# Kernel tuning notes

Hardware: AMD Instinct MI355X
Metric: run time of the kernel (lower is better)

## Reference

```python
import jax, jax.numpy as jnp
import numpy as np

B, E, H = 16384, 768, 8
HD = E // H
EPS = 1e-5


def layernorm(x, g, b):
    m = jnp.mean(x, axis=-1, keepdims=True)
    v = jnp.mean((x - m) ** 2, axis=-1, keepdims=True)
    return (x - m) * jax.lax.rsqrt(v + EPS) * g + b


def mha1(q_in, kv_in, Wq, bq, Wk, bk, Wv, bv, Wo, bo):
    # seq_len-1 cross attention: softmax over a single key is identically 1
    Bn = q_in.shape[0]
    q = (q_in @ Wq.T + bq).reshape(Bn, H, HD)
    k = (kv_in @ Wk.T + bk).reshape(Bn, H, HD)
    v = (kv_in @ Wv.T + bv).reshape(Bn, H, HD)
    scores = jnp.sum(q * k, axis=-1) / (HD ** 0.5)      # [B, H]
    w = jax.nn.softmax(scores[..., None], axis=-1)       # [B, H, 1] == 1
    ctx = (w * v).reshape(Bn, E)
    return ctx @ Wo.T + bo


def ffn(x, W1, b1, W2, b2):
    return jax.nn.gelu(x @ W1.T + b1, approximate=False) @ W2.T + b2


def setup_inputs() -> dict:
    key = jax.random.key(0)
    ks = iter(jax.random.split(key, 40))
    s = 0.02
    d = {
        "image_embed": jax.random.normal(next(ks), (B, E), jnp.float32),
        "text_embed": jax.random.normal(next(ks), (B, E), jnp.float32),
    }
    for p in ("it", "ti"):
        for w in ("Wq", "Wk", "Wv", "Wo"):
            d[f"{p}_{w}"] = jax.random.normal(next(ks), (E, E), jnp.float32) * s
        for bname in ("bq", "bk", "bv", "bo"):
            d[f"{p}_{bname}"] = jnp.zeros((E,), jnp.float32)
    for p in ("ln_img", "ln_text", "fp_ln"):
        d[f"{p}_g"] = jnp.ones((E,), jnp.float32)
        d[f"{p}_b"] = jnp.zeros((E,), jnp.float32)
    for p in ("fi", "ft"):
        d[f"{p}_W1"] = jax.random.normal(next(ks), (4 * E, E), jnp.float32) * s
        d[f"{p}_b1"] = jnp.zeros((4 * E,), jnp.float32)
        d[f"{p}_W2"] = jax.random.normal(next(ks), (E, 4 * E), jnp.float32) * s
        d[f"{p}_b2"] = jnp.zeros((E,), jnp.float32)
    d["fp_W"] = jax.random.normal(next(ks), (E, 2 * E), jnp.float32) * s
    d["fp_b"] = jnp.zeros((E,), jnp.float32)
    return d


def reference(image_embed, text_embed,
              it_Wq, it_Wk, it_Wv, it_Wo, it_bq, it_bk, it_bv, it_bo,
              ti_Wq, ti_Wk, ti_Wv, ti_Wo, ti_bq, ti_bk, ti_bv, ti_bo,
              ln_img_g, ln_img_b, ln_text_g, ln_text_b, fp_ln_g, fp_ln_b,
              fi_W1, fi_b1, fi_W2, fi_b2, ft_W1, ft_b1, ft_W2, ft_b2,
              fp_W, fp_b):
    img_att = mha1(image_embed, text_embed, it_Wq, it_bq, it_Wk, it_bk, it_Wv, it_bv, it_Wo, it_bo)
    img = layernorm(image_embed + img_att, ln_img_g, ln_img_b)
    img = img + ffn(img, fi_W1, fi_b1, fi_W2, fi_b2)
    txt_att = mha1(text_embed, img, ti_Wq, ti_bq, ti_Wk, ti_bk, ti_Wv, ti_bv, ti_Wo, ti_bo)
    txt = layernorm(text_embed + txt_att, ln_text_g, ln_text_b)
    txt = txt + ffn(txt, ft_W1, ft_b1, ft_W2, ft_b2)
    fused = jnp.concatenate([img, txt], axis=-1)
    return jax.nn.gelu(layernorm(fused @ fp_W.T + fp_b, fp_ln_g, fp_ln_b), approximate=False)
```

## Files before the change

### kernel.cpp

```cpp
#include <hip/hip_runtime.h>
#include <hip/hip_bf16.h>
#include <math.h>


typedef unsigned short u16;
typedef __bf16 bf16_t;
typedef bf16_t bf16x8 __attribute__((ext_vector_type(8)));
typedef float f32x4 __attribute__((ext_vector_type(4)));

#define BROWS 16384
#define EDIM  768

__device__ __forceinline__ u16 f2bf(float f) {
    union { float f; unsigned u; } v; v.f = f;
    return (u16)((v.u + 0x7FFFu + ((v.u >> 16) & 1u)) >> 16);
}
__device__ __forceinline__ float bf2f(u16 h) {
    union { unsigned u; float f; } v; v.u = ((unsigned)h) << 16;
    return v.f;
}
__device__ __forceinline__ float gelu_f(float x) {
    float t = x * x;
    float p = fmaf(0.102943268f, t, 2.30221895f);
    float e = __builtin_amdgcn_exp2f(-x * p);
    return x * __builtin_amdgcn_rcpf(1.0f + e);
}

__device__ __forceinline__ void gld16(const u16* g, u16* l) {
    __builtin_amdgcn_global_load_lds(
        (__attribute__((address_space(1))) void*)g,
        (__attribute__((address_space(3))) void*)l, 16, 0, 0);
}

struct ConvBatch {
    const float *s0, *s1, *s2, *s3, *s4, *s5, *s6, *s7;
    u16 *d0, *d1, *d2, *d3, *d4, *d5, *d6, *d7;
};
#define CB0 2304
#define CB1 2304
#define CB2 2304
#define CB3 2304
#define CB4 1152
#define CB5 576
#define CB6 576
#define CB7 12288
#define CONV_BLOCKS (CB0+CB1+CB2+CB3+CB4+CB5+CB6+CB7)

__global__ void __launch_bounds__(256) conv8_k(ConvBatch cb) {
    int b = blockIdx.x;
    const float* s; u16* d;
    if      (b < CB0)          { s = cb.s0; d = cb.d0; }
    else if ((b -= CB0) < CB1) { s = cb.s1; d = cb.d1; }
    else if ((b -= CB1) < CB2) { s = cb.s2; d = cb.d2; }
    else if ((b -= CB2) < CB3) { s = cb.s3; d = cb.d3; }
    else if ((b -= CB3) < CB4) { s = cb.s4; d = cb.d4; }
    else if ((b -= CB4) < CB5) { s = cb.s5; d = cb.d5; }
    else if ((b -= CB5) < CB6) { s = cb.s6; d = cb.d6; }
    else    { b -= CB6;          s = cb.s7; d = cb.d7; }
    int i = b * 256 + threadIdx.x;
    float4 v = ((const float4*)s)[i];
    ushort4 o;
    o.x = f2bf(v.x); o.y = f2bf(v.y); o.z = f2bf(v.z); o.w = f2bf(v.w);
    ((ushort4*)d)[i] = o;
}

__global__ void __launch_bounds__(256) f32_to_bf16_T_k(const float* __restrict__ S,
                                                       u16* __restrict__ D,
                                                       int R, int C) {
    __shared__ float t[32][33];
    const int r0 = blockIdx.y * 32, c0 = blockIdx.x * 32;
    const int tx = threadIdx.x & 31, ty = threadIdx.x >> 5;
#pragma unroll
    for (int i = ty; i < 32; i += 8) t[i][tx] = S[(long)(r0 + i) * C + c0 + tx];
    __syncthreads();
#pragma unroll
    for (int i = ty; i < 32; i += 8) D[(long)(c0 + i) * R + r0 + tx] = f2bf(t[tx][i]);
}

__global__ void __launch_bounds__(256) bias_comb_k(const float* __restrict__ Wo,
                                                   const float* __restrict__ bv,
                                                   const float* __restrict__ bo,
                                                   float* __restrict__ bc, int K) {
    const int n = blockIdx.x * 4 + (threadIdx.x >> 6);
    const int lane = threadIdx.x & 63;
    float s = 0.f;
    for (int k = lane; k < K; k += 64) s += Wo[(long)n * K + k] * bv[k];
#pragma unroll
    for (int o = 32; o > 0; o >>= 1) s += __shfl_down(s, o, 64);
    if (lane == 0) bc[n] = s + bo[n];
}

__global__ void __launch_bounds__(512, 2) gemm_bt(
    const u16* __restrict__ A, int lda,
    const u16* __restrict__ W,
    const float* __restrict__ bias,
    const float* __restrict__ R, int ldr,
    const u16* __restrict__ Rb, int ldrb,
    float* __restrict__ Cf, int ldcf,
    u16* __restrict__ Cb, int ldcb,
    int K, int do_gelu)
{
    __shared__ alignas(16) u16 sA[4][256 * 32];
    __shared__ alignas(16) u16 sB[4][256 * 32];

    const int tid  = threadIdx.x;
    const int lane = tid & 63;
    const int wave = tid >> 6;
    const int wm = wave >> 2;
    const int wn = wave & 3;

    int bm, bn;
    {
        const int gx = gridDim.x, gy = gridDim.y;
        const int id = blockIdx.y * gx + blockIdx.x;
        if ((gy & 7) == 0) {
            const int xcd = id & 7, slot = id >> 3;
            bn = slot % gx;
            bm = (xcd * (gy >> 3)) + slot / gx;
        } else { bm = blockIdx.y; bn = blockIdx.x; }
    }
    const long m0 = (long)bm * 256;
    const long n0 = (long)bn * 256;

    const int srow = lane >> 2;
    const int sk   = ((lane & 3) ^ ((lane >> 3) & 3)) * 8;
    const u16* gA = A + (m0 + wave * 16 + srow) * (long)lda + sk;
    const u16* gB = W + (n0 + wave * 16 + srow) * (long)K + sk;
    const long rdA2 = 128 * (long)lda;
    const long rdB2 = 128 * (long)K;

#define STA(sl, t, ks) do { const u16* g_ = gA + (t) * 64 + (ks) * 32; \
    gld16(g_,        &sA[sl][wave * 512]); \
    gld16(g_ + rdA2, &sA[sl][4096 + wave * 512]); } while (0)
#define STB(sl, t, ks) do { const u16* g_ = gB + (t) * 64 + (ks) * 32; \
    gld16(g_,        &sB[sl][wave * 512]); \
    gld16(g_ + rdB2, &sB[sl][4096 + wave * 512]); } while (0)

    const int quad = lane >> 4;
    const int l16  = lane & 15;
    const int koff = (quad ^ ((l16 >> 1) & 3)) << 4;
    __attribute__((address_space(3))) const u16* baseA3 =
        (__attribute__((address_space(3))) const u16*)
        ((const char*)&sA[0][0] + wm * 8192 + l16 * 64 + koff);
    __attribute__((address_space(3))) const u16* baseB3 =
        (__attribute__((address_space(3))) const u16*)
        ((const char*)&sB[0][0] + wn * 4096 + l16 * 64 + koff);

    f32x4 acc[8][4];
#pragma unroll
    for (int i = 0; i < 8; i++)
#pragma unroll
        for (int j = 0; j < 4; j++) {
            f32x4 z = {0.f, 0.f, 0.f, 0.f};
            acc[i][j] = z;
        }
    bf16x8 af0, af1, af2, af3, bf0, bf1, bf2, bf3;

#define DSR(dst, base, off) \
    asm volatile("ds_read_b128 %0, %1 offset:%2" \
                 : "=v"(dst) : "v"(base), "i"(off))
#define VM4   asm volatile("s_waitcnt vmcnt(4)" ::: "memory")
#define NOWAIT ((void)0)

#define PHASE(SLA, MQ, LB, SLB, STG, WAIT) do {                              \
    DSR(af0, baseA3, (SLA) * 16384 + (MQ) * 4096 + 0);                       \
    DSR(af1, baseA3, (SLA) * 16384 + (MQ) * 4096 + 1024);                    \
    DSR(af2, baseA3, (SLA) * 16384 + (MQ) * 4096 + 2048);                    \
    DSR(af3, baseA3, (SLA) * 16384 + (MQ) * 4096 + 3072);                    \
    if (LB) {                                                                \
        DSR(bf0, baseB3, (SLB) * 16384 + 0);                                 \
        DSR(bf1, baseB3, (SLB) * 16384 + 1024);                              \
        DSR(bf2, baseB3, (SLB) * 16384 + 2048);                              \
        DSR(bf3, baseB3, (SLB) * 16384 + 3072);                              \
    }                                                                        \
    STG;                                                                     \
    WAIT;                                                                    \
    __builtin_amdgcn_sched_barrier(0);                                       \
    __builtin_amdgcn_s_barrier();                                            \
    asm volatile("s_waitcnt lgkmcnt(0)" ::: "memory");                       \
    __builtin_amdgcn_sched_barrier(0);                                       \
    __builtin_amdgcn_s_setprio(1);                                           \
    acc[(MQ)*4+0][0] = __builtin_amdgcn_mfma_f32_16x16x32_bf16(af0, bf0, acc[(MQ)*4+0][0], 0, 0, 0); \
    acc[(MQ)*4+0][1] = __builtin_amdgcn_mfma_f32_16x16x32_bf16(af0, bf1, acc[(MQ)*4+0][1], 0, 0, 0); \
    acc[(MQ)*4+0][2] = __builtin_amdgcn_mfma_f32_16x16x32_bf16(af0, bf2, acc[(MQ)*4+0][2], 0, 0, 0); \
    acc[(MQ)*4+0][3] = __builtin_amdgcn_mfma_f32_16x16x32_bf16(af0, bf3, acc[(MQ)*4+0][3], 0, 0, 0); \
    acc[(MQ)*4+1][0] = __builtin_amdgcn_mfma_f32_16x16x32_bf16(af1, bf0, acc[(MQ)*4+1][0], 0, 0, 0); \
    acc[(MQ)*4+1][1] = __builtin_amdgcn_mfma_f32_16x16x32_bf16(af1, bf1, acc[(MQ)*4+1][1], 0, 0, 0); \
    acc[(MQ)*4+1][2] = __builtin_amdgcn_mfma_f32_16x16x32_bf16(af1, bf2, acc[(MQ)*4+1][2], 0, 0, 0); \
    acc[(MQ)*4+1][3] = __builtin_amdgcn_mfma_f32_16x16x32_bf16(af1, bf3, acc[(MQ)*4+1][3], 0, 0, 0); \
    acc[(MQ)*4+2][0] = __builtin_amdgcn_mfma_f32_16x16x32_bf16(af2, bf0, acc[(MQ)*4+2][0], 0, 0, 0); \
    acc[(MQ)*4+2][1] = __builtin_amdgcn_mfma_f32_16x16x32_bf16(af2, bf1, acc[(MQ)*4+2][1], 0, 0, 0); \
    acc[(MQ)*4+2][2] = __builtin_amdgcn_mfma_f32_16x16x32_bf16(af2, bf2, acc[(MQ)*4+2][2], 0, 0, 0); \
    acc[(MQ)*4+2][3] = __builtin_amdgcn_mfma_f32_16x16x32_bf16(af2, bf3, acc[(MQ)*4+2][3], 0, 0, 0); \
    acc[(MQ)*4+3][0] = __builtin_amdgcn_mfma_f32_16x16x32_bf16(af3, bf0, acc[(MQ)*4+3][0], 0, 0, 0); \
    acc[(MQ)*4+3][1] = __builtin_amdgcn_mfma_f32_16x16x32_bf16(af3, bf1, acc[(MQ)*4+3][1], 0, 0, 0); \
    acc[(MQ)*4+3][2] = __builtin_amdgcn_mfma_f32_16x16x32_bf16(af3, bf2, acc[(MQ)*4+3][2], 0, 0, 0); \
    acc[(MQ)*4+3][3] = __builtin_amdgcn_mfma_f32_16x16x32_bf16(af3, bf3, acc[(MQ)*4+3][3], 0, 0, 0); \
    __builtin_amdgcn_s_setprio(0);                                           \
    __builtin_amdgcn_sched_barrier(0);                                       \
    __builtin_amdgcn_s_barrier();                                            \
  } while (0)

    const int nt = K >> 6;
    STA(0, 0, 0); STB(0, 0, 0);
    STA(1, 0, 1); STB(1, 0, 1);
    STA(2, 1, 0); STB(2, 1, 0);
    VM4;
    __builtin_amdgcn_s_barrier();

    for (int T = 0; T < nt; T += 2) {
        const int t2 = (T + 2 < nt) ? T + 2 : 0;
        const int t3 = (T + 3 < nt) ? T + 3 : 1;
        PHASE(0, 0, 1, 0, STA(3, T + 1, 1), NOWAIT);
        PHASE(0, 1, 0, 0, STB(3, T + 1, 1), VM4);
        PHASE(1, 0, 1, 1, STA(0, t2, 0),    NOWAIT);
        PHASE(1, 1, 0, 1, STB(0, t2, 0),    NOWAIT);
        PHASE(2, 0, 1, 2, STA(1, t2, 1),    NOWAIT);
        PHASE(2, 1, 0, 2, STB(1, t2, 1),    VM4);
        PHASE(3, 0, 1, 3, STA(2, t3, 0),    NOWAIT);
        PHASE(3, 1, 0, 3, STB(2, t3, 0),    NOWAIT);
    }

#pragma unroll
    for (int mt = 0; mt < 8; mt++) {
#pragma unroll
        for (int nf = 0; nf < 4; nf++) {
            const long col = n0 + wn * 64 + nf * 16 + l16;
            const float bv = bias ? bias[col] : 0.0f;
#pragma unroll
            for (int rr = 0; rr < 4; rr++) {
                const long row = m0 + wm * 128 + mt * 16 + quad * 4 + rr;
                float v = acc[mt][nf][rr] + bv;
                if (R)  v += R[row * (long)ldr + col];
                if (Rb) v += bf2f(Rb[row * (long)ldrb + col]);
                if (do_gelu) v = gelu_f(v);
                if (Cf) Cf[row * (long)ldcf + col] = v;
                if (Cb) Cb[row * (long)ldcb + col] = f2bf(v);
            }
        }
    }
#undef PHASE
#undef DSR
#undef STA
#undef STB
#undef VM4
#undef NOWAIT
}

__global__ void __launch_bounds__(256) ln_k(
    const u16*  __restrict__ Xb,
    const float* __restrict__ Xf,
    const float* __restrict__ g,
    const float* __restrict__ b,
    float* __restrict__ Yf,
    u16*   __restrict__ Yb,
    int do_gelu)
{
    const int row = blockIdx.x;
    const int tid = threadIdx.x;
    float v[4] = {0.f, 0.f, 0.f, 0.f};
    if (tid < 192) {
        if (Xb) {
            ushort4 u = ((const ushort4*)(Xb + (long)row * EDIM))[tid];
            v[0] = bf2f(u.x); v[1] = bf2f(u.y); v[2] = bf2f(u.z); v[3] = bf2f(u.w);
        } else {
            float4 f = ((const float4*)(Xf + (long)row * EDIM))[tid];
            v[0] = f.x; v[1] = f.y; v[2] = f.z; v[3] = f.w;
        }
    }
    float s = 0.f, s2 = 0.f;
#pragma unroll
    for (int j = 0; j < 4; j++) { s += v[j]; s2 += v[j] * v[j]; }
#pragma unroll
    for (int o = 32; o > 0; o >>= 1) {
        s  += __shfl_down(s,  o, 64);
        s2 += __shfl_down(s2, o, 64);
    }
    __shared__ float red[8];
    __shared__ float mb[2];
    const int wave = tid >> 6, lane = tid & 63;
    if (lane == 0) { red[wave] = s; red[4 + wave] = s2; }
    __syncthreads();
    if (tid == 0) {
        float S  = red[0] + red[1] + red[2] + red[3];
        float S2 = red[4] + red[5] + red[6] + red[7];
        float mean = S * (1.0f / 768.0f);
        float var  = S2 * (1.0f / 768.0f) - mean * mean;
        mb[0] = mean;
        mb[1] = rsqrtf(var + 1e-5f);
    }
    __syncthreads();
    if (tid < 192) {
        const float mean = mb[0], inv = mb[1];
        float y[4];
#pragma unroll
        for (int j = 0; j < 4; j++) {
            const int c = tid * 4 + j;
            y[j] = (v[j] - mean) * inv * g[c] + b[c];
            if (do_gelu) y[j] = gelu_f(y[j]);
        }
        if (Yf) {
            float4 o = {y[0], y[1], y[2], y[3]};
            ((float4*)(Yf + (long)row * EDIM))[tid] = o;
        }
        if (Yb) {
            ushort4 o = {f2bf(y[0]), f2bf(y[1]), f2bf(y[2]), f2bf(y[3])};
            ((ushort4*)(Yb + (long)row * EDIM))[tid] = o;
        }
    }
}

extern "C" void kernel_launch(void* const* d_in, const int* in_sizes, int n_in,
                              void* d_out, int out_size, void* d_ws, size_t ws_size,
                              hipStream_t stream) {
    (void)in_sizes; (void)n_in; (void)out_size;
    const float* image    = (const float*)d_in[0];
    const float* text     = (const float*)d_in[1];
    const float* it_Wv    = (const float*)d_in[4];
    const float* it_Wo    = (const float*)d_in[5];
    const float* it_bv    = (const float*)d_in[8];
    const float* it_bo    = (const float*)d_in[9];
    const float* ti_Wv    = (const float*)d_in[12];
    const float* ti_Wo    = (const float*)d_in[13];
    const float* ti_bv    = (const float*)d_in[16];
    const float* ti_bo    = (const float*)d_in[17];
    const float* ln_img_g = (const float*)d_in[18];
    const float* ln_img_b = (const float*)d_in[19];
    const float* ln_txt_g = (const float*)d_in[20];
    const float* ln_txt_b = (const float*)d_in[21];
    const float* fp_ln_g  = (const float*)d_in[22];
    const float* fp_ln_b  = (const float*)d_in[23];
    const float* fi_W1    = (const float*)d_in[24];
    const float* fi_b1    = (const float*)d_in[25];
    const float* fi_W2    = (const float*)d_in[26];
    const float* fi_b2    = (const float*)d_in[27];
    const float* ft_W1    = (const float*)d_in[28];
    const float* ft_b1    = (const float*)d_in[29];
    const float* ft_W2    = (const float*)d_in[30];
    const float* ft_b2    = (const float*)d_in[31];
    const float* fp_W     = (const float*)d_in[32];
    const float* fp_b     = (const float*)d_in[33];

    char* ws = (char*)d_ws;
    size_t off = 0;
    auto alloc = [&](size_t bytes) {
        char* p = ws + off; off += (bytes + 255) & ~(size_t)255; return p;
    };
    u16* wo_it = (u16*)alloc((size_t)768 * 768 * 2);
    u16* wvT_it= (u16*)alloc((size_t)768 * 768 * 2);
    u16* wc_it = (u16*)alloc((size_t)768 * 768 * 2);
    u16* wo_ti = (u16*)alloc((size_t)768 * 768 * 2);
    u16* wvT_ti= (u16*)alloc((size_t)768 * 768 * 2);
    u16* wc_ti = (u16*)alloc((size_t)768 * 768 * 2);
    u16* w1i   = (u16*)alloc((size_t)3072 * 768 * 2);
    u16* w2i   = (u16*)alloc((size_t)768 * 3072 * 2);
    u16* w1t   = (u16*)alloc((size_t)3072 * 768 * 2);
    u16* w2t   = (u16*)alloc((size_t)768 * 3072 * 2);
    u16* wp    = (u16*)alloc((size_t)768 * 1536 * 2);
    float* bc_it = (float*)alloc(768 * 4);
    float* bc_ti = (float*)alloc(768 * 4);
    u16* vbuf  = (u16*)alloc((size_t)BROWS * 768 * 2);
    u16* fused = (u16*)alloc((size_t)BROWS * 1536 * 2);
    u16* text_bf = fused;
    int fch = 16384;
    while (fch > 2048 && off + (size_t)fch * 3072 * 2 > ws_size) fch >>= 1;
    size_t region = (size_t)fch * 3072 * 2;
    if (region < (size_t)BROWS * 768 * 2) region = (size_t)BROWS * 768 * 2;
    u16* hbuf = (u16*)alloc(region);
    u16* pbuf = hbuf;

    auto gemm = [&](const u16* A, int lda, const u16* W, int M, int N, int K,
                    const float* bias, const float* R, int ldr,
                    const u16* Rb, int ldrb,
                    float* Cf, int ldcf, u16* Cb, int ldcb, int dg) {
        gemm_bt<<<dim3(N / 256, M / 256), dim3(512), 0, stream>>>(
            A, lda, W, bias, R, ldr, Rb, ldrb, Cf, ldcf, Cb, ldcb, K, dg);
    };
    auto ffn = [&](const u16* xin, const u16* W1, const float* b1,
                   const u16* W2, const float* b2, u16* outp, int ldout) {
        for (int c = 0; c < BROWS / fch; c++) {
            const u16* xc = xin + (size_t)c * fch * 768;
            gemm(xc, 768, W1, fch, 3072, 768, b1,
                 nullptr, 0, nullptr, 0, nullptr, 0, hbuf, 3072, 1);
            gemm(hbuf, 3072, W2, fch, 768, 3072, b2,
                 nullptr, 0, xc, 768,
                 nullptr, 0, outp + (size_t)c * fch * ldout, ldout, 0);
        }
    };

    ConvBatch cbt = { fi_W1, fi_W2, ft_W1, ft_W2, fp_W, it_Wo, ti_Wo, text,
                      w1i,   w2i,   w1t,   w2t,   wp,   wo_it, wo_ti, text_bf };
    conv8_k<<<dim3(CONV_BLOCKS), dim3(256), 0, stream>>>(cbt);
    f32_to_bf16_T_k<<<dim3(24, 24), dim3(256), 0, stream>>>(it_Wv, wvT_it, 768, 768);
    gemm(wo_it, 768, wvT_it, 768, 768, 768, nullptr,
         nullptr, 0, nullptr, 0, nullptr, 0, wc_it, 768, 0);
    bias_comb_k<<<dim3(192), dim3(256), 0, stream>>>(it_Wo, it_bv, it_bo, bc_it, 768);
    f32_to_bf16_T_k<<<dim3(24, 24), dim3(256), 0, stream>>>(ti_Wv, wvT_ti, 768, 768);
    gemm(wo_ti, 768, wvT_ti, 768, 768, 768, nullptr,
         nullptr, 0, nullptr, 0, nullptr, 0, wc_ti, 768, 0);
    bias_comb_k<<<dim3(192), dim3(256), 0, stream>>>(ti_Wo, ti_bv, ti_bo, bc_ti, 768);

    gemm(text_bf, 768, wc_it, BROWS, 768, 768, bc_it,
         image, 768, nullptr, 0, nullptr, 0, pbuf, 768, 0);
    ln_k<<<dim3(BROWS), dim3(256), 0, stream>>>(
        pbuf, nullptr, ln_img_g, ln_img_b, nullptr, vbuf, 0);
    ffn(vbuf, w1i, fi_b1, w2i, fi_b2, fused, 1536);
    gemm(fused, 1536, wc_ti, BROWS, 768, 768, bc_ti,
         text, 768, nullptr, 0, nullptr, 0, pbuf, 768, 0);
    ln_k<<<dim3(BROWS), dim3(256), 0, stream>>>(
        pbuf, nullptr, ln_txt_g, ln_txt_b, nullptr, vbuf, 0);
    ffn(vbuf, w1t, ft_b1, w2t, ft_b2, fused + 768, 1536);
    gemm(fused, 1536, wp, BROWS, 768, 1536, fp_b,
         nullptr, 0, nullptr, 0, nullptr, 0, pbuf, 768, 0);
    ln_k<<<dim3(BROWS), dim3(256), 0, stream>>>(
        pbuf, nullptr, fp_ln_g, fp_ln_b, (float*)d_out, nullptr, 1);
}
```

Before: 1.094 ms.

## Double-buffer LDS fragment registers to overlap ds_reads with MFMA

Restructures the GEMM main loop so the LDS fragment reads for the next phase are issued before the MFMAs of the current phase. Two register sets alternate, and the lgkmcnt/vmcnt waits are partial. Each phase now has one barrier instead of two, which is meant to hide LDS read latency behind matrix math. The cost is higher VGPR pressure from doubled fragment registers, which could lower occupancy. The finer waitcnt accounting also carries a correctness risk if the counts are off.

```diff
diff --git a/kernel.cpp b/kernel.cpp
--- a/kernel.cpp
+++ b/kernel.cpp
@@ -154,72 +154,83 @@
             f32x4 z = {0.f, 0.f, 0.f, 0.f};
             acc[i][j] = z;
         }
-    bf16x8 af0, af1, af2, af3, bf0, bf1, bf2, bf3;
+    bf16x8 a0_0, a0_1, a0_2, a0_3;
+    bf16x8 a1_0, a1_1, a1_2, a1_3;
+    bf16x8 b0_0, b0_1, b0_2, b0_3;
+    bf16x8 b1_0, b1_1, b1_2, b1_3;
 
 #define DSR(dst, base, off) \
     asm volatile("ds_read_b128 %0, %1 offset:%2" \
                  : "=v"(dst) : "v"(base), "i"(off))
-#define VM4   asm volatile("s_waitcnt vmcnt(4)" ::: "memory")
-#define NOWAIT ((void)0)
-
-#define PHASE(SLA, MQ, LB, SLB, STG, WAIT) do {                              \
-    DSR(af0, baseA3, (SLA) * 16384 + (MQ) * 4096 + 0);                       \
-    DSR(af1, baseA3, (SLA) * 16384 + (MQ) * 4096 + 1024);                    \
-    DSR(af2, baseA3, (SLA) * 16384 + (MQ) * 4096 + 2048);                    \
-    DSR(af3, baseA3, (SLA) * 16384 + (MQ) * 4096 + 3072);                    \
-    if (LB) {                                                                \
-        DSR(bf0, baseB3, (SLB) * 16384 + 0);                                 \
-        DSR(bf1, baseB3, (SLB) * 16384 + 1024);                              \
-        DSR(bf2, baseB3, (SLB) * 16384 + 2048);                              \
-        DSR(bf3, baseB3, (SLB) * 16384 + 3072);                              \
-    }                                                                        \
-    STG;                                                                     \
-    WAIT;                                                                    \
-    __builtin_amdgcn_sched_barrier(0);                                       \
-    __builtin_amdgcn_s_barrier();                                            \
-    asm volatile("s_waitcnt lgkmcnt(0)" ::: "memory");                       \
-    __builtin_amdgcn_sched_barrier(0);                                       \
-    __builtin_amdgcn_s_setprio(1);                                           \
-    acc[(MQ)*4+0][0] = __builtin_amdgcn_mfma_f32_16x16x32_bf16(af0, bf0, acc[(MQ)*4+0][0], 0, 0, 0); \
-    acc[(MQ)*4+0][1] = __builtin_amdgcn_mfma_f32_16x16x32_bf16(af0, bf1, acc[(MQ)*4+0][1], 0, 0, 0); \
-    acc[(MQ)*4+0][2] = __builtin_amdgcn_mfma_f32_16x16x32_bf16(af0, bf2, acc[(MQ)*4+0][2], 0, 0, 0); \
-    acc[(MQ)*4+0][3] = __builtin_amdgcn_mfma_f32_16x16x32_bf16(af0, bf3, acc[(MQ)*4+0][3], 0, 0, 0); \
-    acc[(MQ)*4+1][0] = __builtin_amdgcn_mfma_f32_16x16x32_bf16(af1, bf0, acc[(MQ)*4+1][0], 0, 0, 0); \
-    acc[(MQ)*4+1][1] = __builtin_amdgcn_mfma_f32_16x16x32_bf16(af1, bf1, acc[(MQ)*4+1][1], 0, 0, 0); \
-    acc[(MQ)*4+1][2] = __builtin_amdgcn_mfma_f32_16x16x32_bf16(af1, bf2, acc[(MQ)*4+1][2], 0, 0, 0); \
-    acc[(MQ)*4+1][3] = __builtin_amdgcn_mfma_f32_16x16x32_bf16(af1, bf3, acc[(MQ)*4+1][3], 0, 0, 0); \
-    acc[(MQ)*4+2][0] = __builtin_amdgcn_mfma_f32_16x16x32_bf16(af2, bf0, acc[(MQ)*4+2][0], 0, 0, 0); \
-    acc[(MQ)*4+2][1] = __builtin_amdgcn_mfma_f32_16x16x32_bf16(af2, bf1, acc[(MQ)*4+2][1], 0, 0, 0); \
-    acc[(MQ)*4+2][2] = __builtin_amdgcn_mfma_f32_16x16x32_bf16(af2, bf2, acc[(MQ)*4+2][2], 0, 0, 0); \
-    acc[(MQ)*4+2][3] = __builtin_amdgcn_mfma_f32_16x16x32_bf16(af2, bf3, acc[(MQ)*4+2][3], 0, 0, 0); \
-    acc[(MQ)*4+3][0] = __builtin_amdgcn_mfma_f32_16x16x32_bf16(af3, bf0, acc[(MQ)*4+3][0], 0, 0, 0); \
-    acc[(MQ)*4+3][1] = __builtin_amdgcn_mfma_f32_16x16x32_bf16(af3, bf1, acc[(MQ)*4+3][1], 0, 0, 0); \
-    acc[(MQ)*4+3][2] = __builtin_amdgcn_mfma_f32_16x16x32_bf16(af3, bf2, acc[(MQ)*4+3][2], 0, 0, 0); \
-    acc[(MQ)*4+3][3] = __builtin_amdgcn_mfma_f32_16x16x32_bf16(af3, bf3, acc[(MQ)*4+3][3], 0, 0, 0); \
-    __builtin_amdgcn_s_setprio(0);                                           \
-    __builtin_amdgcn_sched_barrier(0);                                       \
-    __builtin_amdgcn_s_barrier();                                            \
+#define RDA(S, SLA, MQ) do { \
+    DSR(a##S##_0, baseA3, (SLA) * 16384 + (MQ) * 4096 + 0);    \
+    DSR(a##S##_1, baseA3, (SLA) * 16384 + (MQ) * 4096 + 1024); \
+    DSR(a##S##_2, baseA3, (SLA) * 16384 + (MQ) * 4096 + 2048); \
+    DSR(a##S##_3, baseA3, (SLA) * 16384 + (MQ) * 4096 + 3072); \
   } while (0)
+#define RDB(S, SLB) do { \
+    DSR(b##S##_0, baseB3, (SLB) * 16384 + 0);    \
+    DSR(b##S##_1, baseB3, (SLB) * 16384 + 1024); \
+    DSR(b##S##_2, baseB3, (SLB) * 16384 + 2048); \
+    DSR(b##S##_3, baseB3, (SLB) * 16384 + 3072); \
+  } while (0)
+
+#define MM16(AS, BS, MQ) do { \
+    acc[(MQ)*4+0][0] = __builtin_amdgcn_mfma_f32_16x16x32_bf16(a##AS##_0, b##BS##_0, acc[(MQ)*4+0][0], 0, 0, 0); \
+    acc[(MQ)*4+0][1] = __builtin_amdgcn_mfma_f32_16x16x32_bf16(a##AS##_0, b##BS##_1, acc[(MQ)*4+0][1], 0, 0, 0); \
+    acc[(MQ)*4+0][2] = __builtin_amdgcn_mfma_f32_16x16x32_bf16(a##AS##_0, b##BS##_2, acc[(MQ)*4+0][2], 0, 0, 0); \
+    acc[(MQ)*4+0][3] = __builtin_amdgcn_mfma_f32_16x16x32_bf16(a##AS##_0, b##BS##_3, acc[(MQ)*4+0][3], 0, 0, 0); \
+    acc[(MQ)*4+1][0] = __builtin_amdgcn_mfma_f32_16x16x32_bf16(a##AS##_1, b##BS##_0, acc[(MQ)*4+1][0], 0, 0, 0); \
+    acc[(MQ)*4+1][1] = __builtin_amdgcn_mfma_f32_16x16x32_bf16(a##AS##_1, b##BS##_1, acc[(MQ)*4+1][1], 0, 0, 0); \
+    acc[(MQ)*4+1][2] = __builtin_amdgcn_mfma_f32_16x16x32_bf16(a##AS##_1, b##BS##_2, acc[(MQ)*4+1][2], 0, 0, 0); \
+    acc[(MQ)*4+1][3] = __builtin_amdgcn_mfma_f32_16x16x32_bf16(a##AS##_1, b##BS##_3, acc[(MQ)*4+1][3], 0, 0, 0); \
+    acc[(MQ)*4+2][0] = __builtin_amdgcn_mfma_f32_16x16x32_bf16(a##AS##_2, b##BS##_0, acc[(MQ)*4+2][0], 0, 0, 0); \
+    acc[(MQ)*4+2][1] = __builtin_amdgcn_mfma_f32_16x16x32_bf16(a##AS##_2, b##BS##_1, acc[(MQ)*4+2][1], 0, 0, 0); \
+    acc[(MQ)*4+2][2] = __builtin_amdgcn_mfma_f32_16x16x32_bf16(a##AS##_2, b##BS##_2, acc[(MQ)*4+2][2], 0, 0, 0); \
+    acc[(MQ)*4+2][3] = __builtin_amdgcn_mfma_f32_16x16x32_bf16(a##AS##_2, b##BS##_3, acc[(MQ)*4+2][3], 0, 0, 0); \
+    acc[(MQ)*4+3][0] = __builtin_amdgcn_mfma_f32_16x16x32_bf16(a##AS##_3, b##BS##_0, acc[(MQ)*4+3][0], 0, 0, 0); \
+    acc[(MQ)*4+3][1] = __builtin_amdgcn_mfma_f32_16x16x32_bf16(a##AS##_3, b##BS##_1, acc[(MQ)*4+3][1], 0, 0, 0); \
+    acc[(MQ)*4+3][2] = __builtin_amdgcn_mfma_f32_16x16x32_bf16(a##AS##_3, b##BS##_2, acc[(MQ)*4+3][2], 0, 0, 0); \
+    acc[(MQ)*4+3][3] = __builtin_amdgcn_mfma_f32_16x16x32_bf16(a##AS##_3, b##BS##_3, acc[(MQ)*4+3][3], 0, 0, 0); \
+  } while (0)
+
+#define PH_TOP0 do { \
+    __builtin_amdgcn_s_barrier(); \
+    __builtin_amdgcn_sched_barrier(0); } while (0)
+#define PH_TOP1 do { \
+    asm volatile("s_waitcnt vmcnt(6)" ::: "memory"); \
+    __builtin_amdgcn_s_barrier(); \
+    __builtin_amdgcn_sched_barrier(0); } while (0)
+#define PH_BOT(LGK, AS, BS, MQ) do { \
+    asm volatile("s_waitcnt lgkmcnt(%0)" :: "i"(LGK) : "memory"); \
+    __builtin_amdgcn_sched_barrier(0); \
+    __builtin_amdgcn_s_setprio(1); \
+    MM16(AS, BS, MQ); \
+    __builtin_amdgcn_s_setprio(0); } while (0)
 
     const int nt = K >> 6;
     STA(0, 0, 0); STB(0, 0, 0);
     STA(1, 0, 1); STB(1, 0, 1);
     STA(2, 1, 0); STB(2, 1, 0);
-    VM4;
+    asm volatile("s_waitcnt vmcnt(8)" ::: "memory");
     __builtin_amdgcn_s_barrier();
+    __builtin_amdgcn_sched_barrier(0);
+    RDA(0, 0, 0); RDB(0, 0);
 
     for (int T = 0; T < nt; T += 2) {
         const int t2 = (T + 2 < nt) ? T + 2 : 0;
         const int t3 = (T + 3 < nt) ? T + 3 : 1;
-        PHASE(0, 0, 1, 0, STA(3, T + 1, 1), NOWAIT);
-        PHASE(0, 1, 0, 0, STB(3, T + 1, 1), VM4);
-        PHASE(1, 0, 1, 1, STA(0, t2, 0),    NOWAIT);
-        PHASE(1, 1, 0, 1, STB(0, t2, 0),    NOWAIT);
-        PHASE(2, 0, 1, 2, STA(1, t2, 1),    NOWAIT);
-        PHASE(2, 1, 0, 2, STB(1, t2, 1),    VM4);
-        PHASE(3, 0, 1, 3, STA(2, t3, 0),    NOWAIT);
-        PHASE(3, 1, 0, 3, STB(2, t3, 0),    NOWAIT);
-    }
+        PH_TOP0; RDA(1, 0, 1);            STA(3, T + 1, 1); PH_BOT(4, 0, 0, 0);
+        PH_TOP1; RDA(0, 1, 0); RDB(1, 1); STB(3, T + 1, 1); PH_BOT(8, 1, 0, 1);
+        PH_TOP0; RDA(1, 1, 1);            STA(0, t2, 0);    PH_BOT(4, 0, 1, 0);
+        PH_TOP1; RDA(0, 2, 0); RDB(0, 2); STB(0, t2, 0);    PH_BOT(8, 1, 1, 1);
+        PH_TOP0; RDA(1, 2, 1);            STA(1, t2, 1);    PH_BOT(4, 0, 0, 0);
+        PH_TOP1; RDA(0, 3, 0); RDB(1, 3); STB(1, t2, 1);    PH_BOT(8, 1, 0, 1);
+        PH_TOP0; RDA(1, 3, 1);            STA(2, t3, 0);    PH_BOT(4, 0, 1, 0);
+        PH_TOP1; RDA(0, 0, 0); RDB(0, 0); STB(2, t3, 0);    PH_BOT(8, 1, 1, 1);
+    }
+    asm volatile("s_waitcnt lgkmcnt(0)" ::: "memory");
+    __builtin_amdgcn_sched_barrier(0);
 
 #pragma unroll
     for (int mt = 0; mt < 8; mt++) {
@@ -239,12 +250,15 @@
             }
         }
     }
-#undef PHASE
+#undef PH_TOP0
+#undef PH_TOP1
+#undef PH_BOT
+#undef MM16
+#undef RDA
+#undef RDB
 #undef DSR
 #undef STA
 #undef STB
-#undef VM4
-#undef NOWAIT
 }
 
 __global__ void __launch_bounds__(256) ln_k(
```

New measurement: 1.096 ms. No clear change (+0.2%).
